# Kernel optimization log

Measured on AMD Instinct MI355X. Metric: run time of the kernel, lower is better.

The kernel has to match this reference:

```python
import jax, jax.numpy as jnp
import numpy as np

N_HEADS = 12
HIDDEN = 768  # NOTE: d_head == hidden_size in this module (unusual)

def setup_inputs() -> dict:
    key = jax.random.key(0)
    ks = jax.random.split(key, 4)
    b, s = 8, 512
    d3 = 3 * N_HEADS * HIDDEN
    return {
        "x": jax.random.normal(ks[0], (b, s, HIDDEN), dtype=jnp.float32),
        "mask": jnp.zeros((b, 1, 1, s), dtype=jnp.float32),
        "w_qkv": jax.random.normal(ks[1], (d3, HIDDEN), dtype=jnp.float32) * 0.02,
        "b_qkv": jnp.zeros((d3,), dtype=jnp.float32),
        "w_o": jax.random.normal(ks[2], (HIDDEN, N_HEADS * HIDDEN), dtype=jnp.float32) * 0.02,
        "b_o": jnp.zeros((HIDDEN,), dtype=jnp.float32),
    }

def reference(x, mask, w_qkv, b_qkv, w_o, b_o):
    b, s, _ = x.shape
    nh = N_HEADS * HIDDEN
    qkv = x @ w_qkv.T + b_qkv                      # (b, s, 3*n*h)
    q, k, v = jnp.split(qkv, 3, axis=-1)           # each (b, s, n*h)
    def heads(t):
        return t.reshape(b, s, N_HEADS, HIDDEN).transpose(0, 2, 1, 3)  # (b, n, s, h)
    q, k, v = heads(q), heads(k), heads(v)
    scale = 1.0 / np.sqrt(HIDDEN).astype(np.float32)
    scores = jnp.einsum('bnqh,bnkh->bnqk', q, k) * scale  # (b, n, s_q, s_k)
    scores = scores + mask                         # additive mask broadcast
    a = jax.nn.softmax(scores, axis=-1)
    av = jnp.einsum('bnqk,bnkh->bnqh', a, v)       # (b, n, s, h)
    h = av.transpose(0, 2, 1, 3).reshape(b, s, nh) # (b, s, n*h)
    return h @ w_o.T + b_o                         # (b, s, hidden)
```

## Files before the change

### kernel.cpp

```cpp
#include <hip/hip_runtime.h>
#include <hip/hip_bf16.h>
#include <stdint.h>

#define AS1 __attribute__((address_space(1)))
#define AS3 __attribute__((address_space(3)))

typedef __attribute__((ext_vector_type(8))) __bf16 bf16x8;
typedef __attribute__((ext_vector_type(16))) float f32x16;
typedef unsigned short u16;
typedef __attribute__((ext_vector_type(8))) unsigned short u16x8;

#define B_    8
#define S_    512
#define NH_   12
#define HD_   768
#define NHD_  (NH_*HD_)
#define D3_   (3*NHD_)
#define QKLD_ (2*NHD_)
#define QK_SCALE 0.03608439182435161f

__device__ __forceinline__ u16 f2bf(float x) {
  union { float f; unsigned u; } a; a.f = x;
  unsigned r = a.u + 0x7fffu + ((a.u >> 16) & 1u);
  return (u16)(r >> 16);
}
__device__ __forceinline__ float bf2f(u16 x) {
  union { unsigned u; float f; } a; a.u = ((unsigned)x) << 16; return a.f;
}
__device__ __forceinline__ uint2 pack4(float a, float b, float c, float d) {
  uint2 r;
  asm("v_cvt_pk_bf16_f32 %0, %1, %2" : "=v"(r.x) : "v"(a), "v"(b));
  asm("v_cvt_pk_bf16_f32 %0, %1, %2" : "=v"(r.y) : "v"(c), "v"(d));
  return r;
}

__device__ __forceinline__ void gload16(const void* g, void* l) {
  __builtin_amdgcn_global_load_lds((const AS1 void*)g, (AS3 void*)l, 16, 0, 0);
}

struct GP {
  const u16* A;
  const u16* B;
  long sAb, sAn, sBb, sBn;
  void* o0; void* o2;
  const float* bias;
  int mMask, mShift, zPerX;
};

template<int MODE, int LDA, int LDB, int KK>
__global__ __launch_bounds__(256)
void gemm_bt(GP p) {
  __shared__ __align__(16) char smem[32768];
  const int tid  = threadIdx.x;
  const int wave = tid >> 6, lane = tid & 63;
  const int wr = wave >> 1, wc = wave & 1;

  int m_idx, n_idx, z;
  {
    const int bid = blockIdx.x;
    const int xcd = bid & 7, loc = bid >> 3;
    if constexpr (MODE == 0) {
      const int mi = loc & p.mMask;
      const int t  = loc >> p.mShift;
      const int n_local = t % 27;
      const int mg = t / 27;
      m_idx = (mg << p.mShift) + mi;
      n_idx = xcd * 27 + n_local;
      z = 0;
    } else if constexpr (MODE == 1) {
      int inner;
      if (p.zPerX) { inner = loc & 15; z = xcd * p.zPerX + (loc >> 4); }
      else         { inner = bid & 15; z = bid >> 4; }
      m_idx = inner >> 2; n_idx = inner & 3;
    } else if constexpr (MODE == 2) {
      int inner;
      if (p.zPerX) { inner = loc % 24; z = xcd * p.zPerX + loc / 24; }
      else         { inner = bid % 24; z = bid / 24; }
      m_idx = inner / 6; n_idx = inner - (inner / 6) * 6;
    } else {
      m_idx = loc & p.mMask;
      n_idx = (xcd & 1) * 3 + (loc >> p.mShift);
      z = xcd >> 1;
    }
  }
  const int bm0 = m_idx * 128, bn0 = n_idx * 128;
  const int zb  = z / NH_, zn = z - zb * NH_;

  const u16* A  = p.A + zb * p.sAb + zn * p.sAn;
  const u16* Bm = p.B + zb * p.sBb + zn * p.sBn;

  f32x16 acc[2][2];
#pragma unroll
  for (int i = 0; i < 2; ++i)
#pragma unroll
    for (int j = 0; j < 2; ++j)
#pragma unroll
      for (int e = 0; e < 16; ++e) acc[i][j][e] = 0.f;

  const int scolsw = ((lane & 7) ^ (lane >> 3)) * 8;
  const u16* gA = A  + (size_t)(bm0 + wave*8 + (lane>>3)) * LDA + scolsw;
  const u16* gB = Bm + (size_t)(bn0 + wave*8 + (lane>>3)) * LDB + scolsw;
  char* ldsA = smem;
  char* ldsB = smem + 16384;
  char* stA  = ldsA + wave*1024;
  char* stB  = ldsB + wave*1024;

  const int aRowB = (wr*64 + (lane & 31)) * 128;
  const int bRowB = (wc*64 + (lane & 31)) * 128;
  const int csw   = lane & 7;
  const int hi    = lane >> 5;

  for (int k0 = 0; k0 < KK; k0 += 64) {
#pragma unroll
    for (int i = 0; i < 4; ++i) {
      gload16(gA + (size_t)i*32*LDA, stA + i*4096);
      gload16(gB + (size_t)i*32*LDB, stB + i*4096);
    }
    gA += 64; gB += 64;
    __syncthreads();
#pragma unroll
    for (int ks = 0; ks < 4; ++ks) {
      const int cOff = ((2*ks + hi) ^ csw) << 4;
      const bf16x8 av0 = *(const bf16x8*)(ldsA + aRowB + cOff);
      const bf16x8 av1 = *(const bf16x8*)(ldsA + aRowB + 4096 + cOff);
      const bf16x8 bv0 = *(const bf16x8*)(ldsB + bRowB + cOff);
      const bf16x8 bv1 = *(const bf16x8*)(ldsB + bRowB + 4096 + cOff);
      acc[0][0] = __builtin_amdgcn_mfma_f32_32x32x16_bf16(bv0, av0, acc[0][0], 0, 0, 0);
      acc[0][1] = __builtin_amdgcn_mfma_f32_32x32x16_bf16(bv1, av0, acc[0][1], 0, 0, 0);
      acc[1][0] = __builtin_amdgcn_mfma_f32_32x32x16_bf16(bv0, av1, acc[1][0], 0, 0, 0);
      acc[1][1] = __builtin_amdgcn_mfma_f32_32x32x16_bf16(bv1, av1, acc[1][1], 0, 0, 0);
    }
    __syncthreads();
  }

  const int mB = bm0 + wr*64 + (lane & 31);
  const int nB = bn0 + wc*64 + (hi << 2);
#pragma unroll
  for (int mi = 0; mi < 2; ++mi) {
    const int m = mB + mi*32;
#pragma unroll
    for (int nj = 0; nj < 2; ++nj) {
#pragma unroll
      for (int q = 0; q < 4; ++q) {
        const int n = nB + nj*32 + 8*q;
        const float v0 = acc[mi][nj][4*q+0];
        const float v1 = acc[mi][nj][4*q+1];
        const float v2 = acc[mi][nj][4*q+2];
        const float v3 = acc[mi][nj][4*q+3];
        if constexpr (MODE == 0) {
          const float4 b4 = *(const float4*)(p.bias + n);
          if (bn0 < QKLD_) {
            *(uint2*)((u16*)p.o0 + (long)m * QKLD_ + n) =
                pack4(v0+b4.x, v1+b4.y, v2+b4.z, v3+b4.w);
          } else {
            const int vcol = n - QKLD_;
            const int nh = vcol / HD_;
            const int h  = vcol - nh * HD_;
            u16* vb = (u16*)p.o2 + (long)((m >> 9) * NH_ + nh) * (S_*HD_)
                      + (long)h * S_ + (m & 511);
            vb[0]    = f2bf(v0+b4.x);
            vb[512]  = f2bf(v1+b4.y);
            vb[1024] = f2bf(v2+b4.z);
            vb[1536] = f2bf(v3+b4.w);
          }
        } else if constexpr (MODE == 1) {
          *(uint2*)((u16*)p.o0 + (long)z*S_*S_ + (long)m*S_ + n) =
              pack4(v0*QK_SCALE, v1*QK_SCALE, v2*QK_SCALE, v3*QK_SCALE);
        } else if constexpr (MODE == 2) {
          *(uint2*)((u16*)p.o0 + (long)(zb*S_ + m)*QKLD_ + zn*HD_ + n) =
              pack4(v0, v1, v2, v3);
        } else {
          const long rowsTot = (long)(p.mMask + 1) * 128;
          float4 f; f.x = v0; f.y = v1; f.z = v2; f.w = v3;
          *(float4*)((float*)p.o0 + ((long)z * rowsTot + m) * HD_ + n) = f;
        }
      }
    }
  }
}

__global__ __launch_bounds__(256)
void softmax_rows(u16* __restrict__ SP, const float* __restrict__ maskc) {
  const int wave = threadIdx.x >> 6, lane = threadIdx.x & 63;
  const int rid = blockIdx.x * 4 + wave;
  const int z = rid >> 9;
  const int b = z / NH_;
  const u16x8 sv = *(const u16x8*)(SP + (size_t)rid * S_ + lane*8);
  const float* mrow = maskc + (size_t)b * S_;
  float vals[8];
  float m = -3.4e38f;
#pragma unroll
  for (int j = 0; j < 8; ++j) {
    vals[j] = bf2f(sv[j]) + mrow[lane*8 + j];
    m = fmaxf(m, vals[j]);
  }
#pragma unroll
  for (int o = 32; o > 0; o >>= 1) m = fmaxf(m, __shfl_xor(m, o));
  float sum = 0.f;
#pragma unroll
  for (int j = 0; j < 8; ++j) { vals[j] = __expf(vals[j] - m); sum += vals[j]; }
#pragma unroll
  for (int o = 32; o > 0; o >>= 1) sum += __shfl_xor(sum, o);
  const float inv = 1.0f / sum;
  u16x8 pv;
#pragma unroll
  for (int j = 0; j < 8; ++j) pv[j] = f2bf(vals[j] * inv);
  *(u16x8*)(SP + (size_t)rid * S_ + lane*8) = pv;
}

__global__ __launch_bounds__(256)
void cvt_bf16(const float4* __restrict__ in, ushort4* __restrict__ out, int n4) {
  const int i = blockIdx.x * 256 + threadIdx.x;
  if (i >= n4) return;
  const float4 v = in[i];
  ushort4 o;
  o.x = f2bf(v.x); o.y = f2bf(v.y); o.z = f2bf(v.z); o.w = f2bf(v.w);
  out[i] = o;
}

__global__ __launch_bounds__(256)
void combine_out(const float4* __restrict__ part, const float* __restrict__ b,
                 float4* __restrict__ out, int n4) {
  const int i = blockIdx.x * 256 + threadIdx.x;
  if (i >= n4) return;
  const float4 a0 = part[i];
  const float4 a1 = part[i + (size_t)n4];
  const float4 a2 = part[i + (size_t)2*n4];
  const float4 a3 = part[i + (size_t)3*n4];
  const int c = (i * 4) % HD_;
  float4 o;
  o.x = a0.x + a1.x + a2.x + a3.x + b[c];
  o.y = a0.y + a1.y + a2.y + a3.y + b[c+1];
  o.z = a0.z + a1.z + a2.z + a3.z + b[c+2];
  o.w = a0.w + a1.w + a2.w + a3.w + b[c+3];
  out[i] = o;
}

extern "C" void kernel_launch(void* const* d_in, const int* in_sizes, int n_in,
                              void* d_out, int out_size, void* d_ws, size_t ws_size,
                              hipStream_t stream) {
  const float* x     = (const float*)d_in[0];
  const float* mask  = (const float*)d_in[1];
  const float* w_qkv = (const float*)d_in[2];
  const float* b_qkv = (const float*)d_in[3];
  const float* w_o   = (const float*)d_in[4];
  const float* b_o   = (const float*)d_in[5];
  float* out = (float*)d_out;

  int bc = 0;
  for (int c = 8; c >= 1; c >>= 1)
    if (56623104UL + (unsigned long)c*35389440UL <= ws_size) { bc = c; break; }
  if (bc == 0) return;

  char* ws = (char*)d_ws;
  u16* wqb = (u16*)(ws);
  u16* wob = (u16*)(ws + 42467328L);
  u16* xb  = (u16*)(ws + 56623104L);
  long off = 56623104L + (long)bc*786432L;
  u16* QKn = (u16*)(ws + off);  off += (long)bc*18874368L;
  u16* Vt  = (u16*)(ws + off);  off += (long)bc*9437184L;
  u16* SP  = (u16*)(ws + off);
  u16* H   = QKn;
  float* Part = (float*)SP;

  cvt_bf16<<<dim3(D3_*HD_/4/256), dim3(256), 0, stream>>>((const float4*)w_qkv, (ushort4*)wqb, D3_*HD_/4);
  cvt_bf16<<<dim3(HD_*NHD_/4/256), dim3(256), 0, stream>>>((const float4*)w_o, (ushort4*)wob, HD_*NHD_/4);

  const int nchunks = B_ / bc;
  const int rows_c = bc * S_;
  const int zc = bc * NH_;
  const int mT = rows_c / 128;
  const int mShift = __builtin_ctz(mT);
  const int MG8 = (mT < 8) ? mT : 8;
  const int mg8Shift = __builtin_ctz(MG8);
  const int zPerX = (zc % 8 == 0) ? zc / 8 : 0;

  for (int c = 0; c < nchunks; ++c) {
    const long row0 = (long)c * rows_c;

    cvt_bf16<<<dim3(rows_c*HD_/4/256), dim3(256), 0, stream>>>(
        (const float4*)(x + row0*HD_), (ushort4*)xb, rows_c*HD_/4);

    GP p1; p1.A = xb; p1.B = wqb;
    p1.sAb = 0; p1.sAn = 0; p1.sBb = 0; p1.sBn = 0;
    p1.o0 = QKn; p1.o2 = Vt; p1.bias = b_qkv;
    p1.mMask = MG8 - 1; p1.mShift = mg8Shift; p1.zPerX = 0;
    gemm_bt<0, HD_, HD_, HD_><<<dim3(216 * mT), dim3(256), 0, stream>>>(p1);

    GP p2; p2.A = QKn; p2.B = QKn + NHD_;
    p2.sAb = (long)S_*QKLD_; p2.sAn = HD_;
    p2.sBb = (long)S_*QKLD_; p2.sBn = HD_;
    p2.o0 = SP; p2.o2 = nullptr; p2.bias = nullptr;
    p2.mMask = 0; p2.mShift = 0; p2.zPerX = zPerX;
    gemm_bt<1, QKLD_, QKLD_, HD_><<<dim3(zc * 16), dim3(256), 0, stream>>>(p2);

    softmax_rows<<<dim3(zc*S_/4), dim3(256), 0, stream>>>(SP, mask + (long)c*bc*S_);

    GP p3; p3.A = SP; p3.B = Vt;
    p3.sAb = (long)NH_*S_*S_; p3.sAn = (long)S_*S_;
    p3.sBb = (long)NH_*S_*HD_; p3.sBn = (long)S_*HD_;
    p3.o0 = H; p3.o2 = nullptr; p3.bias = nullptr;
    p3.mMask = 0; p3.mShift = 0; p3.zPerX = zPerX;
    gemm_bt<2, S_, S_, S_><<<dim3(zc * 24), dim3(256), 0, stream>>>(p3);

    GP p4; p4.A = H; p4.B = wob;
    p4.sAb = 0; p4.sAn = NHD_/4;
    p4.sBb = 0; p4.sBn = NHD_/4;
    p4.o0 = Part; p4.o2 = nullptr; p4.bias = nullptr;
    p4.mMask = mT - 1; p4.mShift = mShift; p4.zPerX = 0;
    gemm_bt<3, QKLD_, NHD_, NHD_/4><<<dim3(24 * mT), dim3(256), 0, stream>>>(p4);

    combine_out<<<dim3(rows_c*HD_/4/256), dim3(256), 0, stream>>>(
        (const float4*)Part, b_o, (float4*)(out + row0*HD_), rows_c*HD_/4);
  }
}
```

Measured before the change: 507.3 us.

## Widen GEMM N-tile to 192 with 6-wave blocks for projection and AV GEMMs

Adds a WN template parameter so three of the four GEMMs use 128x192 output tiles with 384 threads (6 waves in a 2x3 grid), while QK^T keeps 128x128. Tile-to-block mappings and grid sizes are recomputed for the wider N tile, and A/B tile loads are spread across a variable number of waves. The goal is more data reuse per loaded A tile and fewer blocks, which raises LDS use per block and changes occupancy.

```diff
diff --git a/kernel.cpp b/kernel.cpp
--- a/kernel.cpp
+++ b/kernel.cpp
@@ -47,13 +47,13 @@
   int mMask, mShift, zPerX;
 };
 
-template<int MODE, int LDA, int LDB, int KK>
-__global__ __launch_bounds__(256)
+template<int MODE, int LDA, int LDB, int KK, int WN>
+__global__ __launch_bounds__(WN*128, (WN==3) ? 6 : 2)
 void gemm_bt(GP p) {
-  __shared__ __align__(16) char smem[32768];
+  __shared__ __align__(16) char smem[16384 + WN*8192];
   const int tid  = threadIdx.x;
   const int wave = tid >> 6, lane = tid & 63;
-  const int wr = wave >> 1, wc = wave & 1;
+  const int wm = wave & 1, wn = wave >> 1;
 
   int m_idx, n_idx, z;
   {
@@ -62,28 +62,23 @@
     if constexpr (MODE == 0) {
       const int mi = loc & p.mMask;
       const int t  = loc >> p.mShift;
-      const int n_local = t % 27;
-      const int mg = t / 27;
+      const int n_local = t % 18;
+      const int mg = t / 18;
       m_idx = (mg << p.mShift) + mi;
-      n_idx = xcd * 27 + n_local;
+      n_idx = xcd * 18 + n_local;
       z = 0;
-    } else if constexpr (MODE == 1) {
+    } else if constexpr (MODE == 1 || MODE == 2) {
       int inner;
       if (p.zPerX) { inner = loc & 15; z = xcd * p.zPerX + (loc >> 4); }
       else         { inner = bid & 15; z = bid >> 4; }
       m_idx = inner >> 2; n_idx = inner & 3;
-    } else if constexpr (MODE == 2) {
-      int inner;
-      if (p.zPerX) { inner = loc % 24; z = xcd * p.zPerX + loc / 24; }
-      else         { inner = bid % 24; z = bid / 24; }
-      m_idx = inner / 6; n_idx = inner - (inner / 6) * 6;
     } else {
       m_idx = loc & p.mMask;
-      n_idx = (xcd & 1) * 3 + (loc >> p.mShift);
+      n_idx = (xcd & 1) * 2 + (loc >> p.mShift);
       z = xcd >> 1;
     }
   }
-  const int bm0 = m_idx * 128, bn0 = n_idx * 128;
+  const int bm0 = m_idx * 128, bn0 = n_idx * (WN * 64);
   const int zb  = z / NH_, zn = z - zb * NH_;
 
   const u16* A  = p.A + zb * p.sAb + zn * p.sAn;
@@ -98,23 +93,23 @@
       for (int e = 0; e < 16; ++e) acc[i][j][e] = 0.f;
 
   const int scolsw = ((lane & 7) ^ (lane >> 3)) * 8;
-  const u16* gA = A  + (size_t)(bm0 + wave*8 + (lane>>3)) * LDA + scolsw;
-  const u16* gB = Bm + (size_t)(bn0 + wave*8 + (lane>>3)) * LDB + scolsw;
+  const u16* gA = A  + (size_t)(bm0 + (lane>>3)) * LDA + scolsw;
+  const u16* gB = Bm + (size_t)(bn0 + (lane>>3)) * LDB + scolsw;
   char* ldsA = smem;
   char* ldsB = smem + 16384;
-  char* stA  = ldsA + wave*1024;
-  char* stB  = ldsB + wave*1024;
-
-  const int aRowB = (wr*64 + (lane & 31)) * 128;
-  const int bRowB = (wc*64 + (lane & 31)) * 128;
+
+  const int aRowB = (wm*64 + (lane & 31)) * 128;
+  const int bRowB = (wn*64 + (lane & 31)) * 128;
   const int csw   = lane & 7;
   const int hi    = lane >> 5;
 
   for (int k0 = 0; k0 < KK; k0 += 64) {
+    for (int e = wave; e < 16; e += 2*WN)
+      gload16(gA + (size_t)(8*e)*LDA, ldsA + e*1024);
 #pragma unroll
     for (int i = 0; i < 4; ++i) {
-      gload16(gA + (size_t)i*32*LDA, stA + i*4096);
-      gload16(gB + (size_t)i*32*LDB, stB + i*4096);
+      const int e = wave + i*2*WN;
+      gload16(gB + (size_t)(8*e)*LDB, ldsB + e*1024);
     }
     gA += 64; gB += 64;
     __syncthreads();
@@ -133,8 +128,8 @@
     __syncthreads();
   }
 
-  const int mB = bm0 + wr*64 + (lane & 31);
-  const int nB = bn0 + wc*64 + (hi << 2);
+  const int mB = bm0 + wm*64 + (lane & 31);
+  const int nB = bn0 + wn*64 + (hi << 2);
 #pragma unroll
   for (int mi = 0; mi < 2; ++mi) {
     const int m = mB + mi*32;
@@ -285,14 +280,14 @@
     p1.sAb = 0; p1.sAn = 0; p1.sBb = 0; p1.sBn = 0;
     p1.o0 = QKn; p1.o2 = Vt; p1.bias = b_qkv;
     p1.mMask = MG8 - 1; p1.mShift = mg8Shift; p1.zPerX = 0;
-    gemm_bt<0, HD_, HD_, HD_><<<dim3(216 * mT), dim3(256), 0, stream>>>(p1);
+    gemm_bt<0, HD_, HD_, HD_, 3><<<dim3(144 * mT), dim3(384), 0, stream>>>(p1);
 
     GP p2; p2.A = QKn; p2.B = QKn + NHD_;
     p2.sAb = (long)S_*QKLD_; p2.sAn = HD_;
     p2.sBb = (long)S_*QKLD_; p2.sBn = HD_;
     p2.o0 = SP; p2.o2 = nullptr; p2.bias = nullptr;
     p2.mMask = 0; p2.mShift = 0; p2.zPerX = zPerX;
-    gemm_bt<1, QKLD_, QKLD_, HD_><<<dim3(zc * 16), dim3(256), 0, stream>>>(p2);
+    gemm_bt<1, QKLD_, QKLD_, HD_, 2><<<dim3(zc * 16), dim3(256), 0, stream>>>(p2);
 
     softmax_rows<<<dim3(zc*S_/4), dim3(256), 0, stream>>>(SP, mask + (long)c*bc*S_);
 
@@ -301,14 +296,14 @@
     p3.sBb = (long)NH_*S_*HD_; p3.sBn = (long)S_*HD_;
     p3.o0 = H; p3.o2 = nullptr; p3.bias = nullptr;
     p3.mMask = 0; p3.mShift = 0; p3.zPerX = zPerX;
-    gemm_bt<2, S_, S_, S_><<<dim3(zc * 24), dim3(256), 0, stream>>>(p3);
+    gemm_bt<2, S_, S_, S_, 3><<<dim3(zc * 16), dim3(384), 0, stream>>>(p3);
 
     GP p4; p4.A = H; p4.B = wob;
     p4.sAb = 0; p4.sAn = NHD_/4;
     p4.sBb = 0; p4.sBn = NHD_/4;
     p4.o0 = Part; p4.o2 = nullptr; p4.bias = nullptr;
     p4.mMask = mT - 1; p4.mShift = mShift; p4.zPerX = 0;
-    gemm_bt<3, QKLD_, NHD_, NHD_/4><<<dim3(24 * mT), dim3(256), 0, stream>>>(p4);
+    gemm_bt<3, QKLD_, NHD_, NHD_/4, 3><<<dim3(16 * mT), dim3(384), 0, stream>>>(p4);
 
     combine_out<<<dim3(rows_c*HD_/4/256), dim3(256), 0, stream>>>(
         (const float4*)Part, b_o, (float4*)(out + row0*HD_), rows_c*HD_/4);
```

New measurement: 1.424 ms. +180.7%, slower.
